# Kernel optimization log

Hardware: AMD Instinct MI355X
Metric: run time of the kernel (lower is better)

The kernel has to match this reference:

```python
import jax, jax.numpy as jnp
import numpy as np

CMIN, CMAX = -1024.0, 1016.0  # clamp(min=-2**10, max=2**10 - 8) after every op
BRIGHT_F = 1.9   # 1.0 + linspace(0, 0.9, 11)[10]
COLOR_F = 1.9    # 1.0 + linspace(0, 0.9, 11)[10]


def _brightness_dct(x, f):
    # pixel-domain multiplicative brightness; DCT is linear -> scale all coeffs
    return x * f


def _contrast_dct(x, f):
    # pixel contrast: (p - mean)*f + mean.
    # In DCT: AC coeffs scale by f; DC coeff blends toward per-channel mean DC.
    dc_mean = jnp.mean(x[..., 0, 0], axis=(-2, -1), keepdims=True)  # [C,1,1]
    out = x * f
    out = out.at[..., 0, 0].add((1.0 - f) * dc_mean)
    return out


def setup_inputs() -> dict:
    key = jax.random.key(0)
    k1, k2 = jax.random.split(key)
    # luma: [C=1, Hblocks, Wblocks, 8, 8]; chroma 4:2:0: [C=2, H/2, W/2, 8, 8]
    y = jax.random.normal(k1, (1, 512, 512, 8, 8), dtype=jnp.float32) * 100.0
    c = jax.random.normal(k2, (2, 256, 256, 8, 8), dtype=jnp.float32) * 100.0
    return {"y": y, "c": c}


def reference(y, c):
    clamp = lambda t: jnp.clip(t, CMIN, CMAX)
    # dct_prep(mode='start') treated as identity; initial clamp as in forward()
    y = clamp(y)
    c = clamp(c)
    # op 1: Brightness on luma (coeff[0]); both planes clamped after each op
    y = clamp(_brightness_dct(y, BRIGHT_F))
    c = clamp(c)
    # op 2: Color = contrast on chroma (coeff[1])
    c = clamp(_contrast_dct(c, COLOR_F))
    y = clamp(y)
    # dct_prep(mode='end') treated as identity
    return y, c
```

## Files before the change

### kernel.cpp

```cpp
#include <hip/hip_runtime.h>

#define CMIN -1024.0f
#define CMAX 1016.0f

__device__ __forceinline__ float clampv(float x) {
    return fminf(fmaxf(x, CMIN), CMAX);
}

__device__ __forceinline__ float wave_reduce(float v) {
    #pragma unroll
    for (int off = 32; off > 0; off >>= 1)
        v += __shfl_down(v, off, 64);
    return v;
}

__global__ void __launch_bounds__(256)
y_and_dc(const float4* __restrict__ y4, const float* __restrict__ c,
         float4* __restrict__ out, float* __restrict__ ws,
         int ynvec, int dc_count)
{
    const int tid = blockIdx.x * blockDim.x + threadIdx.x;
    __shared__ float smem[4];

    float dcv = 0.0f;
    if (tid < dc_count) dcv = clampv(c[(size_t)tid * 64]);

    if (tid < ynvec) {
        float4 v = y4[tid];
        v.x = clampv(clampv(v.x) * 1.9f);
        v.y = clampv(clampv(v.y) * 1.9f);
        v.z = clampv(clampv(v.z) * 1.9f);
        v.w = clampv(clampv(v.w) * 1.9f);
        out[tid] = v;
    }

    if (blockIdx.x < (dc_count >> 8)) {
        float s = wave_reduce(dcv);
        const int lane = threadIdx.x & 63;
        const int wave = threadIdx.x >> 6;
        if (lane == 0) smem[wave] = s;
        __syncthreads();
        if (threadIdx.x == 0)
            ws[blockIdx.x] = smem[0] + smem[1] + smem[2] + smem[3];
    }
}

__global__ void __launch_bounds__(256)
c_elementwise(const float4* __restrict__ c4, float4* __restrict__ outc,
              const float* __restrict__ ws, int cnvec, int c_half_nvec,
              float neg09_inv_count)
{
    const int i = blockIdx.x * blockDim.x + threadIdx.x;
    __shared__ float sm[8];
    __shared__ float sadj[2];

    float4 v;
    if (i < cnvec) v = c4[i];

    float s0 = wave_reduce(ws[threadIdx.x]);
    float s1 = wave_reduce(ws[256 + threadIdx.x]);
    const int lane = threadIdx.x & 63;
    const int wave = threadIdx.x >> 6;
    if (lane == 0) { sm[wave] = s0; sm[4 + wave] = s1; }
    __syncthreads();
    if (threadIdx.x == 0) {
        sadj[0] = (sm[0] + sm[1] + sm[2] + sm[3]) * neg09_inv_count;
        sadj[1] = (sm[4] + sm[5] + sm[6] + sm[7]) * neg09_inv_count;
    }
    __syncthreads();

    if (i < cnvec) {
        float4 r;
        r.x = clampv(v.x) * 1.9f;
        r.y = clampv(v.y) * 1.9f;
        r.z = clampv(v.z) * 1.9f;
        r.w = clampv(v.w) * 1.9f;
        if ((i & 15) == 0)
            r.x += (i < c_half_nvec) ? sadj[0] : sadj[1];
        r.x = clampv(r.x);
        r.y = clampv(r.y);
        r.z = clampv(r.z);
        r.w = clampv(r.w);
        outc[i] = r;
    }
}

extern "C" void kernel_launch(void* const* d_in, const int* in_sizes, int n_in,
                              void* d_out, int out_size, void* d_ws, size_t ws_size,
                              hipStream_t stream) {
    const float* y = (const float*)d_in[0];
    const float* c = (const float*)d_in[1];
    float* out = (float*)d_out;
    float* ws  = (float*)d_ws;

    const int yN = in_sizes[0];
    const int cN = in_sizes[1];

    const int ynvec       = yN / 4;
    const int cnvec       = cN / 4;
    const int c_half_nvec = cnvec / 2;
    const int dc_count    = cN / 64;
    const float neg09_inv_count = -0.9f / (float)(dc_count / 2);

    y_and_dc<<<(ynvec + 255) / 256, 256, 0, stream>>>(
        (const float4*)y, c, (float4*)out, ws, ynvec, dc_count);

    c_elementwise<<<(cnvec + 255) / 256, 256, 0, stream>>>(
        (const float4*)c, (float4*)out + ynvec, ws, cnvec, c_half_nvec,
        neg09_inv_count);
}
```

Baseline: 180.6 us.

## Process chroma in one pass and patch DC coefficients in a small fixup kernel

Merges the luma and chroma elementwise work into a single streaming kernel. The chroma blocks write their clamped-scaled outputs directly, save the pre-adjust DC values, and emit per-block DC partial sums. A second small kernel reduces all the partials and rewrites only the DC coefficients. This removes the second full pass over the chroma data and the strided DC gather, at the cost of a redundant partial reduction in every fixup block and a scattered DC write.

```diff
diff --git a/kernel.cpp b/kernel.cpp
--- a/kernel.cpp
+++ b/kernel.cpp
@@ -14,16 +14,13 @@
     return v;
 }
 
+
 __global__ void __launch_bounds__(256)
-y_and_dc(const float4* __restrict__ y4, const float* __restrict__ c,
-         float4* __restrict__ out, float* __restrict__ ws,
-         int ynvec, int dc_count)
+payload_kernel(const float4* __restrict__ y4, const float4* __restrict__ c4,
+               float4* __restrict__ out, float* __restrict__ partials,
+               float* __restrict__ dcbuf, int ynvec, int yblocks)
 {
     const int tid = blockIdx.x * blockDim.x + threadIdx.x;
-    __shared__ float smem[4];
-
-    float dcv = 0.0f;
-    if (tid < dc_count) dcv = clampv(c[(size_t)tid * 64]);
 
     if (tid < ynvec) {
         float4 v = y4[tid];
@@ -32,33 +29,56 @@
         v.z = clampv(clampv(v.z) * 1.9f);
         v.w = clampv(clampv(v.w) * 1.9f);
         out[tid] = v;
-    }
+    } else {
+        const int ic = tid - ynvec;
+        float4 v = c4[ic];
+        float4 r;
+        r.x = clampv(v.x) * 1.9f;
+        r.y = clampv(v.y) * 1.9f;
+        r.z = clampv(v.z) * 1.9f;
+        r.w = clampv(v.w) * 1.9f;
 
-    if (blockIdx.x < (dc_count >> 8)) {
+        float dcv = 0.0f;
+        if ((ic & 15) == 0) {
+            dcv = clampv(v.x);
+            dcbuf[ic >> 4] = r.x;
+        }
+        r.x = clampv(r.x);
+        r.y = clampv(r.y);
+        r.z = clampv(r.z);
+        r.w = clampv(r.w);
+        out[tid] = r;
+
+        __shared__ float smem[4];
         float s = wave_reduce(dcv);
         const int lane = threadIdx.x & 63;
         const int wave = threadIdx.x >> 6;
         if (lane == 0) smem[wave] = s;
         __syncthreads();
         if (threadIdx.x == 0)
-            ws[blockIdx.x] = smem[0] + smem[1] + smem[2] + smem[3];
+            partials[blockIdx.x - yblocks] = smem[0] + smem[1] + smem[2] + smem[3];
     }
 }
 
 __global__ void __launch_bounds__(256)
-c_elementwise(const float4* __restrict__ c4, float4* __restrict__ outc,
-              const float* __restrict__ ws, int cnvec, int c_half_nvec,
-              float neg09_inv_count)
+dc_fixup(float* __restrict__ outf, const float* __restrict__ partials,
+         const float* __restrict__ dcbuf, int dc_per_ch,
+         float neg09_inv_count)
 {
-    const int i = blockIdx.x * blockDim.x + threadIdx.x;
+    const int d = blockIdx.x * blockDim.x + threadIdx.x;
+
+    const float pre = dcbuf[d];
+
+    float s0 = 0.0f, s1 = 0.0f;
+    for (int j = threadIdx.x; j < 4096; j += 256) {
+        s0 += partials[j];
+        s1 += partials[4096 + j];
+    }
+    s0 = wave_reduce(s0);
+    s1 = wave_reduce(s1);
+
     __shared__ float sm[8];
     __shared__ float sadj[2];
-
-    float4 v;
-    if (i < cnvec) v = c4[i];
-
-    float s0 = wave_reduce(ws[threadIdx.x]);
-    float s1 = wave_reduce(ws[256 + threadIdx.x]);
     const int lane = threadIdx.x & 63;
     const int wave = threadIdx.x >> 6;
     if (lane == 0) { sm[wave] = s0; sm[4 + wave] = s1; }
@@ -69,20 +89,8 @@
     }
     __syncthreads();
 
-    if (i < cnvec) {
-        float4 r;
-        r.x = clampv(v.x) * 1.9f;
-        r.y = clampv(v.y) * 1.9f;
-        r.z = clampv(v.z) * 1.9f;
-        r.w = clampv(v.w) * 1.9f;
-        if ((i & 15) == 0)
-            r.x += (i < c_half_nvec) ? sadj[0] : sadj[1];
-        r.x = clampv(r.x);
-        r.y = clampv(r.y);
-        r.z = clampv(r.z);
-        r.w = clampv(r.w);
-        outc[i] = r;
-    }
+    const float adj = (d < dc_per_ch) ? sadj[0] : sadj[1];
+    outf[(size_t)d * 64] = clampv(pre + adj);
 }
 
 extern "C" void kernel_launch(void* const* d_in, const int* in_sizes, int n_in,
@@ -96,16 +104,21 @@
     const int yN = in_sizes[0];
     const int cN = in_sizes[1];
 
-    const int ynvec       = yN / 4;
-    const int cnvec       = cN / 4;
-    const int c_half_nvec = cnvec / 2;
-    const int dc_count    = cN / 64;
-    const float neg09_inv_count = -0.9f / (float)(dc_count / 2);
+    const int ynvec    = yN / 4;
+    const int cnvec    = cN / 4;
+    const int yblocks  = ynvec / 256;
+    const int cblocks  = cnvec / 256;
+    const int dc_count = cN / 64;
+    const int dc_per_ch = dc_count / 2;
+    const float neg09_inv_count = -0.9f / (float)dc_per_ch;
 
-    y_and_dc<<<(ynvec + 255) / 256, 256, 0, stream>>>(
-        (const float4*)y, c, (float4*)out, ws, ynvec, dc_count);
+    float* partials = ws;
+    float* dcbuf    = ws + 8192;
 
-    c_elementwise<<<(cnvec + 255) / 256, 256, 0, stream>>>(
-        (const float4*)c, (float4*)out + ynvec, ws, cnvec, c_half_nvec,
-        neg09_inv_count);
+    payload_kernel<<<yblocks + cblocks, 256, 0, stream>>>(
+        (const float4*)y, (const float4*)c, (float4*)out, partials, dcbuf,
+        ynvec, yblocks);
+
+    dc_fixup<<<dc_count / 256, 256, 0, stream>>>(
+        out + (size_t)yN, partials, dcbuf, dc_per_ch, neg09_inv_count);
 }
```

Result: no change. 180.8 us (+0.1%).
